# Optimization experiments

Measured on AMD Instinct MI355X. Metric: run time of the kernel, lower is better.

Reference implementation:

```python
import jax, jax.numpy as jnp
import numpy as np

H = 768
NH = 12
HD = 64
FF = 3072
EPS = 1e-12


def layer_norm(x, g, b):
    mu = jnp.mean(x, axis=-1, keepdims=True)
    var = jnp.mean((x - mu) ** 2, axis=-1, keepdims=True)
    return (x - mu) * jax.lax.rsqrt(var + EPS) * g + b


def setup_inputs() -> dict:
    key = jax.random.key(0)
    ks = jax.random.split(key, 16)
    B, S, L = 16, 512, 50
    s = 0.02
    return {
        "hidden_states": jax.random.normal(ks[0], (B, S, H), jnp.float32),
        "attention_mask": jnp.zeros((B, 1, 1, S), jnp.float32),
        "past_key": jax.random.normal(ks[1], (B, NH, L, HD), jnp.float32),
        "past_value": jax.random.normal(ks[2], (B, NH, L, HD), jnp.float32),
        "Wq": jax.random.normal(ks[3], (H, H), jnp.float32) * s,
        "bq": jnp.zeros((H,), jnp.float32),
        "Wk": jax.random.normal(ks[4], (H, H), jnp.float32) * s,
        "bk": jnp.zeros((H,), jnp.float32),
        "Wv": jax.random.normal(ks[5], (H, H), jnp.float32) * s,
        "bv": jnp.zeros((H,), jnp.float32),
        "Wo": jax.random.normal(ks[6], (H, H), jnp.float32) * s,
        "bo": jnp.zeros((H,), jnp.float32),
        "ln1_g": jnp.ones((H,), jnp.float32),
        "ln1_b": jnp.zeros((H,), jnp.float32),
        "Wi": jax.random.normal(ks[7], (H, FF), jnp.float32) * s,
        "bi": jnp.zeros((FF,), jnp.float32),
        "Wf": jax.random.normal(ks[8], (FF, H), jnp.float32) * s,
        "bf": jnp.zeros((H,), jnp.float32),
        "ln2_g": jnp.ones((H,), jnp.float32),
        "ln2_b": jnp.zeros((H,), jnp.float32),
    }


def reference(hidden_states, attention_mask, past_key, past_value,
              Wq, bq, Wk, bk, Wv, bv, Wo, bo, ln1_g, ln1_b,
              Wi, bi, Wf, bf, ln2_g, ln2_b):
    B, S, _ = hidden_states.shape
    L = past_key.shape[2]

    def heads(x):  # [B,S,H] -> [B,NH,S,HD]
        return x.reshape(B, S, NH, HD).transpose(0, 2, 1, 3)

    q = heads(hidden_states @ Wq + bq)
    k = heads(hidden_states @ Wk + bk)
    v = heads(hidden_states @ Wv + bv)

    # faithful to source bug: past_key_values[0] concatenated into BOTH k and v
    k = jnp.concatenate([past_key, k], axis=2)  # [B,NH,L+S,HD]
    v = jnp.concatenate([past_key, v], axis=2)

    scores = jnp.einsum('bhqd,bhkd->bhqk', q, k) / jnp.sqrt(jnp.float32(HD))
    # visual mask positions get +1.0 (torch.ones), faithful to source
    vis_mask = jnp.ones((B, 1, 1, L), scores.dtype)
    full_mask = jnp.concatenate([vis_mask, attention_mask], axis=-1)
    scores = scores + full_mask

    probs = jax.nn.softmax(scores, axis=-1)
    ctx = jnp.einsum('bhqk,bhkd->bhqd', probs, v)  # [B,NH,S,HD]
    ctx = ctx.transpose(0, 2, 1, 3).reshape(B, S, H)

    attn_out = layer_norm(ctx @ Wo + bo + hidden_states, ln1_g, ln1_b)

    inter = jax.nn.gelu(attn_out @ Wi + bi, approximate=False)
    layer_out = layer_norm(inter @ Wf + bf + attn_out, ln2_g, ln2_b)
    return layer_out
```

## Files before the change

### kernel.cpp

```cpp
#include <hip/hip_runtime.h>
#include <math.h>

#define HDIM 64
#define NHEAD 12
#define HDN 768
#define QKVN 2304
#define FFDIM 3072
#define LPAST 50
#define SEQ 512
#define NBATCH 16
#define TKV (LPAST + SEQ)
#define TKVP 576
#define MTOK (NBATCH * SEQ)
#define NBH (NBATCH * NHEAD)

typedef __attribute__((ext_vector_type(8))) short short8;
typedef __attribute__((ext_vector_type(4))) float f32x4;

__device__ __forceinline__ ushort f2bf(float x) {
    union { float f; unsigned u; } c; c.f = x;
    unsigned r = (c.u + 0x7fffu + ((c.u >> 16) & 1u)) >> 16;
    return (ushort)r;
}
__device__ __forceinline__ float bf2f(ushort u) { return __uint_as_float((unsigned)u << 16); }
__device__ __forceinline__ float geluf(float v) {
    return 0.5f * v * (1.0f + erff(v * 0.70710678118654752f));
}
__device__ __forceinline__ float gelu_fast(float v) {
    float u = 0.7978845608f * v * fmaf(0.044715f * v, v, 1.0f);
    float e = __expf(2.0f * u);
    float th = 1.0f - 2.0f / (e + 1.0f);
    return 0.5f * v * (1.0f + th);
}

#define GLOAD_LDS16(gsrc, ldst)                                                    \
    __builtin_amdgcn_global_load_lds(                                              \
        (const __attribute__((address_space(1))) void*)(gsrc),                     \
        (__attribute__((address_space(3))) void*)(ldst), 16, 0, 0)

__global__ __launch_bounds__(256) void prep(
    const float* __restrict__ hs, ushort* __restrict__ hs_bf,
    const float* __restrict__ bq, const float* __restrict__ bk,
    const float* __restrict__ bv, float* __restrict__ bqkv,
    const float* __restrict__ Wq, const float* __restrict__ Wk,
    const float* __restrict__ Wv, const float* __restrict__ Wo,
    ushort* __restrict__ WqT, ushort* __restrict__ WkT,
    ushort* __restrict__ WvT, ushort* __restrict__ WoT,
    const float* __restrict__ Wi, ushort* __restrict__ WiT,
    const float* __restrict__ Wf, ushort* __restrict__ WfT)
{
    __shared__ float tls[32][33];
    int bid = blockIdx.x;
    const int tid = threadIdx.x;

    if (bid < 6144) {
        int i = bid * 256 + tid;
        float4 v = ((const float4*)hs)[i];
        ushort4 o; o.x = f2bf(v.x); o.y = f2bf(v.y); o.z = f2bf(v.z); o.w = f2bf(v.w);
        ((ushort4*)hs_bf)[i] = o;
        return;
    }
    bid -= 6144;
    if (bid < 9) {
        int i = bid * 256 + tid;
        bqkv[i] = i < HDN ? bq[i] : (i < 2 * HDN ? bk[i - HDN] : bv[i - 2 * HDN]);
        return;
    }
    bid -= 9;

    const float* W; ushort* WT; int K, N, bx, by;
    if (bid < 2304) {
        int z = bid / 576, r = bid % 576;
        W = z == 0 ? Wq : z == 1 ? Wk : z == 2 ? Wv : Wo;
        WT = z == 0 ? WqT : z == 1 ? WkT : z == 2 ? WvT : WoT;
        K = HDN; N = HDN; bx = r % 24; by = r / 24;
    } else if (bid < 4608) {
        int r = bid - 2304; W = Wi; WT = WiT; K = HDN; N = FFDIM; bx = r % 96; by = r / 96;
    } else {
        int r = bid - 4608; W = Wf; WT = WfT; K = FFDIM; N = HDN; bx = r % 24; by = r / 24;
    }
    const int n0 = bx * 32, k0 = by * 32;
    const int tx = tid & 31, ty = tid >> 5;
    #pragma unroll
    for (int i = 0; i < 4; ++i)
        tls[ty + i * 8][tx] = W[(size_t)(k0 + ty + i * 8) * N + n0 + tx];
    __syncthreads();
    #pragma unroll
    for (int i = 0; i < 4; ++i)
        WT[(size_t)(n0 + ty + i * 8) * K + k0 + tx] = f2bf(tls[tx][ty + i * 8]);
}

template<int EPI, int BN>
__global__ __launch_bounds__(256, BN == 64 ? 3 : 2) void gemm_t(
    const ushort* __restrict__ A, const ushort* __restrict__ B,
    int lda, int ldb,
    const float* __restrict__ bias, const float* __restrict__ resid,
    const ushort* __restrict__ resid_bf,
    ushort* __restrict__ Cout, int M, int N, int K)
{
    constexpr int NF = BN / 32;
    constexpr int NBL = BN / 32;
    constexpr int BHS = BN * 4;
    constexpr int BHU = BN * 32;
    constexpr int BUFU = 8192 + BN * 64;
    __shared__ ushort sm[2 * BUFU];

    const int tid = threadIdx.x;
    const int lane = tid & 63;
    const int wv = tid >> 6;
    const int wr = wv >> 1, wc = wv & 1;
    const int bm = blockIdx.x * 128, bn = blockIdx.y * BN;
    const int lr = lane & 15, lg = lane >> 4;
    const int swzu = ((lr * 64 + lg * 16) ^ ((lr & 8) << 2)) >> 1;
    const size_t kzoff = (size_t)blockIdx.z * K;

    int arow[4], akk[4], brow[NBL], bkk[NBL];
    #pragma unroll
    for (int r = 0; r < 4; ++r) {
        int sl = tid + 256 * r;
        int half = sl >> 9, within = sl & 511;
        int o = within * 16;
        int st = o >> 10, q = o & 1023;
        q ^= ((q >> 9) & 1) << 5;
        arow[r] = st * 16 + (q >> 6);
        akk[r] = half * 32 + ((q & 63) >> 1);
    }
    #pragma unroll
    for (int r = 0; r < NBL; ++r) {
        int sl = tid + 256 * r;
        int half = sl / BHS, within = sl % BHS;
        int o = within * 16;
        int st = o >> 10, q = o & 1023;
        q ^= ((q >> 9) & 1) << 5;
        brow[r] = st * 16 + (q >> 6);
        bkk[r] = half * 32 + ((q & 63) >> 1);
    }
    const ushort* Abase = A + (size_t)bm * lda + kzoff;
    const ushort* Bbase = B + (size_t)bn * ldb + kzoff;
    const int nt = K >> 6;

    f32x4 acc[4][NF] = {};

#define STAGE(T, BUF)                                                            \
    do {                                                                         \
        const int k0_ = (T) << 6;                                                \
        char* base_ = (char*)(sm + (BUF) * BUFU);                                \
        _Pragma("unroll")                                                        \
        for (int r_ = 0; r_ < 4; ++r_)                                           \
            GLOAD_LDS16(Abase + (size_t)arow[r_] * lda + k0_ + akk[r_],          \
                        base_ + (tid + 256 * r_) * 16);                          \
        _Pragma("unroll")                                                        \
        for (int r_ = 0; r_ < NBL; ++r_)                                         \
            GLOAD_LDS16(Bbase + (size_t)brow[r_] * ldb + k0_ + bkk[r_],          \
                        base_ + 16384 + (tid + 256 * r_) * 16);                  \
    } while (0)

    STAGE(0, 0);
    asm volatile("s_waitcnt vmcnt(0)" ::: "memory");
    __builtin_amdgcn_sched_barrier(0);
    __builtin_amdgcn_s_barrier();
    __builtin_amdgcn_sched_barrier(0);

    int buf = 0;
    for (int t = 0; t < nt; ++t) {
        if (t + 1 < nt) STAGE(t + 1, buf ^ 1);
        const ushort* ab = sm + buf * BUFU;
        short8 af[4][2], bfv[NF][2];
        #pragma unroll
        for (int i = 0; i < 4; ++i)
            #pragma unroll
            for (int h = 0; h < 2; ++h)
                af[i][h] = *(const short8*)(ab + h * 4096 + (wr * 4 + i) * 512 + swzu);
        #pragma unroll
        for (int j = 0; j < NF; ++j)
            #pragma unroll
            for (int h = 0; h < 2; ++h)
                bfv[j][h] = *(const short8*)(ab + 8192 + h * BHU + (wc * NF + j) * 512 + swzu);
        __builtin_amdgcn_s_setprio(1);
        #pragma unroll
        for (int i = 0; i < 4; ++i)
            #pragma unroll
            for (int j = 0; j < NF; ++j) {
                acc[i][j] = __builtin_amdgcn_mfma_f32_16x16x32_bf16(
                    bfv[j][0], af[i][0], acc[i][j], 0, 0, 0);
                acc[i][j] = __builtin_amdgcn_mfma_f32_16x16x32_bf16(
                    bfv[j][1], af[i][1], acc[i][j], 0, 0, 0);
            }
        __builtin_amdgcn_s_setprio(0);
        asm volatile("s_waitcnt vmcnt(0)" ::: "memory");
        __builtin_amdgcn_sched_barrier(0);
        __builtin_amdgcn_s_barrier();
        __builtin_amdgcn_sched_barrier(0);
        buf ^= 1;
    }
#undef STAGE

    ushort* Cz = Cout + (size_t)blockIdx.z * M * N;
    #pragma unroll
    for (int i = 0; i < 4; ++i) {
        const int row = bm + wr * 64 + i * 16 + lr;
        #pragma unroll
        for (int j = 0; j < NF; ++j) {
            const int col = bn + wc * (BN / 2) + j * 16 + lg * 4;
            const size_t idx = (size_t)row * N + col;
            float v0 = acc[i][j][0], v1 = acc[i][j][1],
                  v2 = acc[i][j][2], v3 = acc[i][j][3];
            if (EPI != 5) {
                float4 b4 = *(const float4*)&bias[col];
                v0 += b4.x; v1 += b4.y; v2 += b4.z; v3 += b4.w;
            }
            if (EPI == 1) {
                float4 r4 = *(const float4*)&resid[idx];
                v0 += r4.x; v1 += r4.y; v2 += r4.z; v3 += r4.w;
            }
            if (EPI == 4) {
                ushort4 rb = *(const ushort4*)&resid_bf[idx];
                v0 += bf2f(rb.x); v1 += bf2f(rb.y);
                v2 += bf2f(rb.z); v3 += bf2f(rb.w);
            }
            if (EPI == 2) {
                v0 = gelu_fast(v0); v1 = gelu_fast(v1);
                v2 = gelu_fast(v2); v3 = gelu_fast(v3);
            }
            ushort4 o;
            o.x = f2bf(v0); o.y = f2bf(v1); o.z = f2bf(v2); o.w = f2bf(v3);
            *(ushort4*)&Cz[idx] = o;
        }
    }
}

__global__ __launch_bounds__(256) void kvAll(
    const ushort* __restrict__ qkv, const float* __restrict__ past_key,
    ushort* __restrict__ kf, ushort* __restrict__ vt)
{
    __shared__ ushort td[64][72];
    const int bh = blockIdx.x / 9;
    const int t0 = (blockIdx.x % 9) * 64;
    const int b = bh / NHEAD, h = bh % NHEAD;
    const int trow = threadIdx.x >> 2, seg = threadIdx.x & 3;
    const int t = t0 + trow;

    ushort kv16[16], vv16[16];
    if (t < LPAST) {
        const float* pk = past_key + ((size_t)bh * LPAST + t) * HDIM + seg * 16;
        #pragma unroll
        for (int i = 0; i < 4; ++i) {
            float4 f = ((const float4*)pk)[i];
            kv16[i * 4 + 0] = f2bf(f.x); kv16[i * 4 + 1] = f2bf(f.y);
            kv16[i * 4 + 2] = f2bf(f.z); kv16[i * 4 + 3] = f2bf(f.w);
        }
        #pragma unroll
        for (int i = 0; i < 16; ++i) vv16[i] = kv16[i];
    } else if (t < TKV) {
        const ushort* kp = qkv + ((size_t)(b * SEQ + (t - LPAST))) * QKVN
                               + HDN + h * HDIM + seg * 16;
        *(uint4*)&kv16[0] = ((const uint4*)kp)[0];
        *(uint4*)&kv16[8] = ((const uint4*)kp)[1];
        const ushort* vp = kp + HDN;
        *(uint4*)&vv16[0] = ((const uint4*)vp)[0];
        *(uint4*)&vv16[8] = ((const uint4*)vp)[1];
    } else {
        #pragma unroll
        for (int i = 0; i < 16; ++i) { kv16[i] = 0; vv16[i] = 0; }
    }

    if (t < TKV) {
        ushort* kd = kf + (((size_t)bh * TKV + t) << 6) + seg * 16;
        *(uint4*)kd = *(uint4*)&kv16[0];
        *(uint4*)(kd + 8) = *(uint4*)&kv16[8];
    }

    #pragma unroll
    for (int i = 0; i < 16; ++i) td[trow][seg * 16 + i] = vv16[i];
    __syncthreads();

    const int d = threadIdx.x >> 2;
    ushort o[16];
    #pragma unroll
    for (int i = 0; i < 16; ++i) o[i] = td[seg * 16 + i][d];
    ushort* dst = vt + ((size_t)bh * HDIM + d) * TKVP + t0 + seg * 16;
    *(uint4*)dst = *(uint4*)&o[0];
    *(uint4*)(dst + 8) = *(uint4*)&o[8];
}

__global__ __launch_bounds__(256) void attn4(
    const ushort* __restrict__ qkv, const ushort* __restrict__ kf,
    const ushort* __restrict__ vt, const float* __restrict__ mask,
    ushort* __restrict__ ctx)
{
    __shared__ ushort Ks[64 * 64];
    __shared__ ushort Vs[64 * 64];
    __shared__ ushort Ps[4][16 * 64];

    const int wv = threadIdx.x >> 6, lane = threadIdx.x & 63;
    const int lr = lane & 15, lg = lane >> 4;
    const int bid = blockIdx.x;
    const int xcd = bid & 7, gi = bid >> 3;
    const int bh = xcd * (NBH / 8) + (gi >> 3);
    const int s0 = (gi & 7) * 64;
    const int b = bh / NHEAD, h = bh % NHEAD;

    short8 af[2];
    {
        const ushort* qp = qkv + ((size_t)(b * SEQ + s0 + wv * 16 + lr)) * QKVN
                               + h * HDIM + lg * 8;
        af[0] = *(const short8*)qp;
        af[1] = *(const short8*)(qp + 32);
    }

    const ushort* kbase = kf + (size_t)bh * TKV * HDIM;
    const ushort* vbase = vt + (size_t)bh * HDIM * TKVP;

    float l[4] = {};
    f32x4 ctxa[4] = {};

    for (int kt = 0; kt < 9; ++kt) {
        const int t0 = kt * 64;
        #pragma unroll
        for (int r = 0; r < 2; ++r) {
            int sl = (int)threadIdx.x + 256 * r;
            int row = sl >> 3, p = sl & 7;
            int j = p ^ (row & 7);
            int trow = t0 + row; if (trow > TKV - 1) trow = TKV - 1;
            GLOAD_LDS16(kbase + ((size_t)trow << 6) + j * 8, (char*)Ks + sl * 16);
        }
        #pragma unroll
        for (int r = 0; r < 2; ++r) {
            int sl = (int)threadIdx.x + 256 * r;
            int row = sl >> 3, p = sl & 7;
            int j = p ^ (row & 7);
            GLOAD_LDS16(vbase + (size_t)row * TKVP + t0 + j * 8, (char*)Vs + sl * 16);
        }
        __syncthreads();

        f32x4 sa[4] = {};
        #pragma unroll
        for (int kb = 0; kb < 4; ++kb) {
            const int key = kb * 16 + lr;
            #pragma unroll
            for (int c = 0; c < 2; ++c) {
                const int phys = (c * 4 + lg) ^ (key & 7);
                short8 kfrag = *(const short8*)&Ks[key * 64 + phys * 8];
                sa[kb] = __builtin_amdgcn_mfma_f32_16x16x32_bf16(
                    af[c], kfrag, sa[kb], 0, 0, 0);
            }
        }

        #pragma unroll
        for (int kb = 0; kb < 4; ++kb) {
            const int t = t0 + kb * 16 + lr;
            float addv;
            if (t >= TKV) addv = -1e30f;
            else addv = ((t < LPAST) ? 1.0f : mask[(size_t)b * SEQ + (t - LPAST)]) - 4.0f;
            const int key = kb * 16 + lr;
            #pragma unroll
            for (int r = 0; r < 4; ++r) {
                float p = __expf(fmaf(sa[kb][r], 0.125f, addv));
                l[r] += p;
                const int q_ = lg * 4 + r;
                const int phys = (key >> 3) ^ (q_ & 7);
                Ps[wv][q_ * 64 + phys * 8 + (key & 7)] = f2bf(p);
            }
        }

        short8 pa[2];
        #pragma unroll
        for (int c = 0; c < 2; ++c) {
            const int phys = (c * 4 + lg) ^ (lr & 7);
            pa[c] = *(const short8*)&Ps[wv][lr * 64 + phys * 8];
        }
        #pragma unroll
        for (int dg = 0; dg < 4; ++dg) {
            const int d = dg * 16 + lr;
            #pragma unroll
            for (int c = 0; c < 2; ++c) {
                const int phys = (c * 4 + lg) ^ (d & 7);
                short8 vfrag = *(const short8*)&Vs[d * 64 + phys * 8];
                ctxa[dg] = __builtin_amdgcn_mfma_f32_16x16x32_bf16(
                    pa[c], vfrag, ctxa[dg], 0, 0, 0);
            }
        }
        __syncthreads();
    }

    #pragma unroll
    for (int r = 0; r < 4; ++r) {
        float s = l[r];
        s += __shfl_xor(s, 1); s += __shfl_xor(s, 2);
        s += __shfl_xor(s, 4); s += __shfl_xor(s, 8);
        l[r] = 1.0f / s;
    }
    #pragma unroll
    for (int r = 0; r < 4; ++r) {
        const int q_ = s0 + wv * 16 + lg * 4 + r;
        const size_t base = ((size_t)(b * SEQ + q_)) * HDN + h * HDIM;
        #pragma unroll
        for (int dg = 0; dg < 4; ++dg)
            ctx[base + dg * 16 + lr] = f2bf(ctxa[dg][r] * l[r]);
    }
}

__global__ __launch_bounds__(256) void layernorm3(
    const ushort* __restrict__ x, const float* __restrict__ g,
    const float* __restrict__ b, float* __restrict__ out,
    ushort* __restrict__ out_bf)
{
    const size_t row = blockIdx.x;
    const ushort* xr = &x[row * HDN];
    const int t = threadIdx.x;

    float v0 = bf2f(xr[t]), v1 = bf2f(xr[t + 256]), v2 = bf2f(xr[t + 512]);

    __shared__ float red[4];
    float s = v0 + v1 + v2;
    #pragma unroll
    for (int off = 32; off > 0; off >>= 1) s += __shfl_xor(s, off);
    if ((t & 63) == 0) red[t >> 6] = s;
    __syncthreads();
    float mean = (red[0] + red[1] + red[2] + red[3]) * (1.0f / 768.0f);

    float d0 = v0 - mean, d1 = v1 - mean, d2 = v2 - mean;
    float vs = d0 * d0 + d1 * d1 + d2 * d2;
    #pragma unroll
    for (int off = 32; off > 0; off >>= 1) vs += __shfl_xor(vs, off);
    __syncthreads();
    if ((t & 63) == 0) red[t >> 6] = vs;
    __syncthreads();
    float var = (red[0] + red[1] + red[2] + red[3]) * (1.0f / 768.0f);
    float rstd = rsqrtf(var + 1e-12f);

    float o0 = d0 * rstd * g[t] + b[t];
    float o1 = d1 * rstd * g[t + 256] + b[t + 256];
    float o2 = d2 * rstd * g[t + 512] + b[t + 512];
    if (out) {
        out[row * HDN + t] = o0;
        out[row * HDN + t + 256] = o1;
        out[row * HDN + t + 512] = o2;
    }
    if (out_bf) {
        out_bf[row * HDN + t] = f2bf(o0);
        out_bf[row * HDN + t + 256] = f2bf(o1);
        out_bf[row * HDN + t + 512] = f2bf(o2);
    }
}

__global__ __launch_bounds__(256) void ln_red(
    const ushort* __restrict__ p0, const ushort* __restrict__ p1,
    const float* __restrict__ bias, const ushort* __restrict__ resid,
    const float* __restrict__ g, const float* __restrict__ b,
    float* __restrict__ out)
{
    const size_t row = blockIdx.x;
    const size_t base = row * HDN;
    const int t = threadIdx.x;

    float v0 = bf2f(p0[base + t])       + bf2f(p1[base + t])       + bias[t]       + bf2f(resid[base + t]);
    float v1 = bf2f(p0[base + t + 256]) + bf2f(p1[base + t + 256]) + bias[t + 256] + bf2f(resid[base + t + 256]);
    float v2 = bf2f(p0[base + t + 512]) + bf2f(p1[base + t + 512]) + bias[t + 512] + bf2f(resid[base + t + 512]);

    __shared__ float red[4];
    float s = v0 + v1 + v2;
    #pragma unroll
    for (int off = 32; off > 0; off >>= 1) s += __shfl_xor(s, off);
    if ((t & 63) == 0) red[t >> 6] = s;
    __syncthreads();
    float mean = (red[0] + red[1] + red[2] + red[3]) * (1.0f / 768.0f);

    float d0 = v0 - mean, d1 = v1 - mean, d2 = v2 - mean;
    float vs = d0 * d0 + d1 * d1 + d2 * d2;
    #pragma unroll
    for (int off = 32; off > 0; off >>= 1) vs += __shfl_xor(vs, off);
    __syncthreads();
    if ((t & 63) == 0) red[t >> 6] = vs;
    __syncthreads();
    float var = (red[0] + red[1] + red[2] + red[3]) * (1.0f / 768.0f);
    float rstd = rsqrtf(var + 1e-12f);

    out[base + t]       = d0 * rstd * g[t]       + b[t];
    out[base + t + 256] = d1 * rstd * g[t + 256] + b[t + 256];
    out[base + t + 512] = d2 * rstd * g[t + 512] + b[t + 512];
}

extern "C" void kernel_launch(void* const* d_in, const int* in_sizes, int n_in,
                              void* d_out, int out_size, void* d_ws, size_t ws_size,
                              hipStream_t stream) {
    const float* hs       = (const float*)d_in[0];
    const float* mask     = (const float*)d_in[1];
    const float* past_key = (const float*)d_in[2];
    const float* Wq = (const float*)d_in[4];
    const float* bq = (const float*)d_in[5];
    const float* Wk = (const float*)d_in[6];
    const float* bk = (const float*)d_in[7];
    const float* Wv = (const float*)d_in[8];
    const float* bv = (const float*)d_in[9];
    const float* Wo = (const float*)d_in[10];
    const float* bo = (const float*)d_in[11];
    const float* ln1_g = (const float*)d_in[12];
    const float* ln1_b = (const float*)d_in[13];
    const float* Wi = (const float*)d_in[14];
    const float* bi = (const float*)d_in[15];
    const float* Wf = (const float*)d_in[16];
    const float* bf_ = (const float*)d_in[17];
    const float* ln2_g = (const float*)d_in[18];
    const float* ln2_b = (const float*)d_in[19];
    float* out = (float*)d_out;

    char* w = (char*)d_ws;
    ushort* WqT   = (ushort*)(w + 0);
    ushort* WoT   = (ushort*)(w + 3538944);
    ushort* WiT   = (ushort*)(w + 4718592);
    ushort* WfT   = (ushort*)(w + 9437184);
    float*  bqkv  = (float*)(w + 14155776);
    ushort* hs_bf = (ushort*)(w + 14172160);
    ushort* qkv   = (ushort*)(w + 26755072);
    ushort* kf    = (ushort*)(w + 64503808);
    ushort* vt    = (ushort*)(w + 78315520);
    ushort* ctx_bf = hs_bf;
    ushort* tmp_bf = (ushort*)(w + 64503808);
    ushort* inter  = (ushort*)(w + 14172160);
    ushort* pbuf   = (ushort*)(w + 64503808);
    ushort* aln_bf = (ushort*)(w + 89669632);
    ushort* WkT = WqT + (size_t)HDN * HDN;
    ushort* WvT = WqT + (size_t)2 * HDN * HDN;

    dim3 b256(256);

    prep<<<dim3(13065), b256, 0, stream>>>(
        hs, hs_bf, bq, bk, bv, bqkv,
        Wq, Wk, Wv, Wo, WqT, WkT, WvT, WoT, Wi, WiT, Wf, WfT);

    gemm_t<0, 128><<<dim3(MTOK / 128, QKVN / 128), b256, 0, stream>>>(
        hs_bf, WqT, HDN, HDN, bqkv, nullptr, nullptr, qkv, MTOK, QKVN, HDN);

    kvAll<<<dim3(NBH * 9), b256, 0, stream>>>(qkv, past_key, kf, vt);

    attn4<<<dim3(NBH * 8), b256, 0, stream>>>(qkv, kf, vt, mask, ctx_bf);

    gemm_t<1, 64><<<dim3(MTOK / 128, HDN / 64), b256, 0, stream>>>(
        ctx_bf, WoT, HDN, HDN, bo, hs, nullptr, tmp_bf, MTOK, HDN, HDN);
    layernorm3<<<dim3(MTOK), b256, 0, stream>>>(tmp_bf, ln1_g, ln1_b, nullptr, aln_bf);

    gemm_t<2, 128><<<dim3(MTOK / 128, FFDIM / 128), b256, 0, stream>>>(
        aln_bf, WiT, HDN, HDN, bi, nullptr, nullptr, inter, MTOK, FFDIM, HDN);
    gemm_t<5, 128><<<dim3(MTOK / 128, HDN / 128, 2), b256, 0, stream>>>(
        inter, WfT, FFDIM, FFDIM, nullptr, nullptr, nullptr, pbuf, MTOK, HDN, FFDIM / 2);

    ln_red<<<dim3(MTOK), b256, 0, stream>>>(
        pbuf, pbuf + (size_t)MTOK * HDN, bf_, aln_bf, ln2_g, ln2_b, out);
}
```

Before: 244.8 us.

## Halve GEMM K-tile to 32 and raise occupancy in launch bounds

Cuts the per-stage K depth of the bf16 MFMA GEMM from 64 to 32, which halves LDS buffer size and fragment registers, and raises the launch-bounds occupancy targets from 3/2 to 6/5 blocks per CU. The aim is to hide global-to-LDS latency with more resident waves. In exchange there are twice as many barrier-synchronised iterations, each with less MFMA work to cover the loads. An unused erf GELU helper is also removed.

Result: slower. 552.6 us (+125.8%).

```diff
diff --git a/kernel.cpp b/kernel.cpp
--- a/kernel.cpp
+++ b/kernel.cpp
@@ -23,9 +23,6 @@
     return (ushort)r;
 }
 __device__ __forceinline__ float bf2f(ushort u) { return __uint_as_float((unsigned)u << 16); }
-__device__ __forceinline__ float geluf(float v) {
-    return 0.5f * v * (1.0f + erff(v * 0.70710678118654752f));
-}
 __device__ __forceinline__ float gelu_fast(float v) {
     float u = 0.7978845608f * v * fmaf(0.044715f * v, v, 1.0f);
     float e = __expf(2.0f * u);
@@ -91,7 +88,7 @@
 }
 
 template<int EPI, int BN>
-__global__ __launch_bounds__(256, BN == 64 ? 3 : 2) void gemm_t(
+__global__ __launch_bounds__(256, BN == 64 ? 6 : 5) void gemm_t(
     const ushort* __restrict__ A, const ushort* __restrict__ B,
     int lda, int ldb,
     const float* __restrict__ bias, const float* __restrict__ resid,
@@ -99,10 +96,8 @@
     ushort* __restrict__ Cout, int M, int N, int K)
 {
     constexpr int NF = BN / 32;
-    constexpr int NBL = BN / 32;
-    constexpr int BHS = BN * 4;
-    constexpr int BHU = BN * 32;
-    constexpr int BUFU = 8192 + BN * 64;
+    constexpr int NBG = BN / 64;
+    constexpr int BUFU = 4096 + BN * 32;
     __shared__ ushort sm[2 * BUFU];
 
     const int tid = threadIdx.x;
@@ -114,45 +109,41 @@
     const int swzu = ((lr * 64 + lg * 16) ^ ((lr & 8) << 2)) >> 1;
     const size_t kzoff = (size_t)blockIdx.z * K;
 
-    int arow[4], akk[4], brow[NBL], bkk[NBL];
-    #pragma unroll
-    for (int r = 0; r < 4; ++r) {
-        int sl = tid + 256 * r;
-        int half = sl >> 9, within = sl & 511;
-        int o = within * 16;
+    int arow[2], akk[2], brow[NBG], bkk[NBG];
+    #pragma unroll
+    for (int r = 0; r < 2; ++r) {
+        int o = (tid + 256 * r) * 16;
         int st = o >> 10, q = o & 1023;
         q ^= ((q >> 9) & 1) << 5;
         arow[r] = st * 16 + (q >> 6);
-        akk[r] = half * 32 + ((q & 63) >> 1);
-    }
-    #pragma unroll
-    for (int r = 0; r < NBL; ++r) {
-        int sl = tid + 256 * r;
-        int half = sl / BHS, within = sl % BHS;
-        int o = within * 16;
+        akk[r] = (q & 63) >> 1;
+    }
+    #pragma unroll
+    for (int r = 0; r < NBG; ++r) {
+        int o = (tid + 256 * r) * 16;
         int st = o >> 10, q = o & 1023;
         q ^= ((q >> 9) & 1) << 5;
         brow[r] = st * 16 + (q >> 6);
-        bkk[r] = half * 32 + ((q & 63) >> 1);
+        bkk[r] = (q & 63) >> 1;
     }
     const ushort* Abase = A + (size_t)bm * lda + kzoff;
     const ushort* Bbase = B + (size_t)bn * ldb + kzoff;
-    const int nt = K >> 6;
+    const int nt = K >> 5;
 
     f32x4 acc[4][NF] = {};
 
 #define STAGE(T, BUF)                                                            \
     do {                                                                         \
-        const int k0_ = (T) << 6;                                                \
+        const int k0_ = (T) << 5;                                                \
         char* base_ = (char*)(sm + (BUF) * BUFU);                                \
         _Pragma("unroll")                                                        \
-        for (int r_ = 0; r_ < 4; ++r_)                                           \
+        for (int r_ = 0; r_ < 2; ++r_)                                           \
             GLOAD_LDS16(Abase + (size_t)arow[r_] * lda + k0_ + akk[r_],          \
                         base_ + (tid + 256 * r_) * 16);                          \
         _Pragma("unroll")                                                        \
-        for (int r_ = 0; r_ < NBL; ++r_)                                         \
+        for (int r_ = 0; r_ < NBG; ++r_)                                         \
             GLOAD_LDS16(Bbase + (size_t)brow[r_] * ldb + k0_ + bkk[r_],          \
-                        base_ + 16384 + (tid + 256 * r_) * 16);                  \
+                        base_ + 8192 + (tid + 256 * r_) * 16);                   \
     } while (0)
 
     STAGE(0, 0);
@@ -165,27 +156,20 @@
     for (int t = 0; t < nt; ++t) {
         if (t + 1 < nt) STAGE(t + 1, buf ^ 1);
         const ushort* ab = sm + buf * BUFU;
-        short8 af[4][2], bfv[NF][2];
+        short8 af[4], bfv[NF];
+        #pragma unroll
+        for (int i = 0; i < 4; ++i)
+            af[i] = *(const short8*)(ab + (wr * 4 + i) * 512 + swzu);
+        #pragma unroll
+        for (int j = 0; j < NF; ++j)
+            bfv[j] = *(const short8*)(ab + 4096 + (wc * NF + j) * 512 + swzu);
+        __builtin_amdgcn_s_setprio(1);
         #pragma unroll
         for (int i = 0; i < 4; ++i)
             #pragma unroll
-            for (int h = 0; h < 2; ++h)
-                af[i][h] = *(const short8*)(ab + h * 4096 + (wr * 4 + i) * 512 + swzu);
-        #pragma unroll
-        for (int j = 0; j < NF; ++j)
-            #pragma unroll
-            for (int h = 0; h < 2; ++h)
-                bfv[j][h] = *(const short8*)(ab + 8192 + h * BHU + (wc * NF + j) * 512 + swzu);
-        __builtin_amdgcn_s_setprio(1);
-        #pragma unroll
-        for (int i = 0; i < 4; ++i)
-            #pragma unroll
-            for (int j = 0; j < NF; ++j) {
+            for (int j = 0; j < NF; ++j)
                 acc[i][j] = __builtin_amdgcn_mfma_f32_16x16x32_bf16(
-                    bfv[j][0], af[i][0], acc[i][j], 0, 0, 0);
-                acc[i][j] = __builtin_amdgcn_mfma_f32_16x16x32_bf16(
-                    bfv[j][1], af[i][1], acc[i][j], 0, 0, 0);
-            }
+                    bfv[j], af[i], acc[i][j], 0, 0, 0);
         __builtin_amdgcn_s_setprio(0);
         asm volatile("s_waitcnt vmcnt(0)" ::: "memory");
         __builtin_amdgcn_sched_barrier(0);
```
